# Kernel tuning notes

Hardware: AMD Instinct MI355X
Metric: run time of the kernel (lower is better)

Reference implementation:

```python
import jax, jax.numpy as jnp
import numpy as np

B, S, D, H, DH = 2, 2048, 1024, 16, 64  # batch, seq, d_hidden, n_head, d_head


def setup_inputs() -> dict:
    key = jax.random.key(0)
    ks = jax.random.split(key, 11)
    sc = 0.02
    inp = {
        "Q": jax.random.normal(ks[0], (B, S, D), jnp.float32),
        "K": jax.random.normal(ks[1], (B, S, D), jnp.float32),
        "V": jax.random.normal(ks[2], (B, S, D), jnp.float32),
        # causal mask: True = masked (strictly upper triangular), broadcast to [B,S,S]
        "attn_mask": jnp.broadcast_to(jnp.triu(jnp.ones((S, S), bool), k=1), (B, S, S)),
        "W_q": jax.random.normal(ks[3], (H * DH, D), jnp.float32) * sc,
        "b_q": jnp.zeros((H * DH,), jnp.float32),
        "W_k": jax.random.normal(ks[4], (H * DH, D), jnp.float32) * sc,
        "b_k": jnp.zeros((H * DH,), jnp.float32),
        "W_v": jax.random.normal(ks[5], (H * DH, D), jnp.float32) * sc,
        "b_v": jnp.zeros((H * DH,), jnp.float32),
        "W_o": jax.random.normal(ks[6], (D, H * DH), jnp.float32) * sc,
        "b_o": jnp.zeros((D,), jnp.float32),
    }
    return inp


def reference(Q, K, V, attn_mask, W_q, b_q, W_k, b_k, W_v, b_v, W_o, b_o):
    scaler = 1.0 / (DH ** 0.5)
    # projections: torch Linear is x @ W.T + b
    def proj(x, W, b):
        y = jnp.einsum('bsd,ed->bse', x, W) + b  # e = H*DH
        return y.reshape(x.shape[0], x.shape[1], H, DH).transpose(0, 2, 1, 3)  # [B,H,S,DH]
    q = proj(Q, W_q, b_q)
    k = proj(K, W_k, b_k)
    v = proj(V, W_v, b_v)
    score = jnp.einsum('bhqd,bhkd->bhqk', q, k) * scaler
    score = jnp.where(attn_mask[:, None, :, :], jnp.float32(-1e9), score)
    attn_prob = jax.nn.softmax(score, axis=-1)  # dropout p=0.0 -> identity
    context = jnp.einsum('bhqk,bhkd->bhqd', attn_prob, v)
    context = context.transpose(0, 2, 1, 3).reshape(Q.shape[0], -1, H * DH)
    output = jnp.einsum('bse,de->bsd', context, W_o) + b_o
    return (output, attn_prob)
```

## Files before the change

kernel.cpp:

```cpp
#include <hip/hip_runtime.h>
#include <hip/hip_bf16.h>

typedef __attribute__((ext_vector_type(8))) __bf16 bf16x8;
typedef __attribute__((ext_vector_type(4))) float f32x4;
typedef __attribute__((ext_vector_type(4))) float f4;

#define MB 2
#define MS 2048
#define MD 1024
#define MH 16
#define MDH 64

__device__ __forceinline__ void gl_lds16(const __bf16* g, __bf16* l) {
  __builtin_amdgcn_global_load_lds(
      (const __attribute__((address_space(1))) unsigned int*)g,
      (__attribute__((address_space(3))) unsigned int*)l, 16, 0, 0);
}

__device__ __forceinline__ void stage64(const __bf16* __restrict__ g, int gstride,
                                        __bf16* lds, int t) {
#pragma unroll
  for (int j = 0; j < 2; j++) {
    const int slot = t + j * 256;
    const int r = slot >> 3;
    const int c = (slot & 7) ^ (r & 7);
    gl_lds16(g + (size_t)r * gstride + c * 8, &lds[slot * 8]);
  }
}

__device__ __forceinline__ bf16x8 frag_ld(const __bf16* lds, int row, int kc) {
  const int slot = row * 8 + (kc ^ (row & 7));
  return *(const bf16x8*)&lds[slot * 8];
}

__global__ __launch_bounds__(256) void convert_kernel(
    const float* __restrict__ Q, const float* __restrict__ K, const float* __restrict__ V,
    const float* __restrict__ Wq, const float* __restrict__ Wk, const float* __restrict__ Wv,
    const float* __restrict__ Wo, __bf16* __restrict__ Ab, __bf16* __restrict__ Wb) {
  const size_t base = ((size_t)blockIdx.x * 256 + threadIdx.x) * 8;
  const float* src;
  __bf16* dst;
  size_t off;
  if (base < 3UL * 4194304UL) {
    const int z = (int)(base >> 22);
    off = base & 4194303UL;
    src = (z == 0) ? Q : ((z == 1) ? K : V);
    dst = Ab + ((size_t)z << 22);
  } else {
    const size_t b2 = base - 3UL * 4194304UL;
    const int w = (int)(b2 >> 20);
    off = b2 & 1048575UL;
    src = (w == 0) ? Wq : ((w == 1) ? Wk : ((w == 2) ? Wv : Wo));
    dst = Wb + ((size_t)w << 20);
  }
  f4 a = *(const f4*)(src + off);
  f4 b = *(const f4*)(src + off + 4);
  bf16x8 o;
#pragma unroll
  for (int j = 0; j < 4; j++) {
    o[j] = (__bf16)a[j];
    o[j + 4] = (__bf16)b[j];
  }
  *(bf16x8*)(dst + off) = o;
}

__device__ __forceinline__ void gemm_core(const __bf16* __restrict__ A,
                                          const __bf16* __restrict__ W,
                                          int tile_m, int tile_n,
                                          f32x4 acc[4][4]) {
  __shared__ __bf16 a_lds[8192];
  __shared__ __bf16 w_lds[8192];
  const int t = threadIdx.x;
  const int lane = t & 63, wave = t >> 6;
  const int l15 = lane & 15, quad = lane >> 4;
  const int wr = wave >> 1, wc = wave & 1;

  const f32x4 fzero = {0.f, 0.f, 0.f, 0.f};
#pragma unroll
  for (int mi = 0; mi < 4; mi++)
#pragma unroll
    for (int ni = 0; ni < 4; ni++) acc[mi][ni] = fzero;

  const __bf16* Abase = A + (size_t)(tile_m * 128) * 1024;
  const __bf16* Wbase = W + (size_t)(tile_n * 128) * 1024;

  for (int k0 = 0; k0 < 1024; k0 += 64) {
    __syncthreads();
#pragma unroll
    for (int j = 0; j < 4; j++) {
      const int slot = t + j * 256;
      const int r = slot >> 3;
      const int c = (slot & 7) ^ (r & 7);
      gl_lds16(Abase + (size_t)r * 1024 + k0 + c * 8, &a_lds[slot * 8]);
    }
#pragma unroll
    for (int j = 0; j < 4; j++) {
      const int slot = t + j * 256;
      const int r = slot >> 3;
      const int c = (slot & 7) ^ (r & 7);
      gl_lds16(Wbase + (size_t)r * 1024 + k0 + c * 8, &w_lds[slot * 8]);
    }
    __syncthreads();

#pragma unroll
    for (int kk = 0; kk < 2; kk++) {
      bf16x8 af[4], bf[4];
#pragma unroll
      for (int mi = 0; mi < 4; mi++)
        af[mi] = frag_ld(a_lds, wr * 64 + mi * 16 + l15, kk * 4 + quad);
#pragma unroll
      for (int ni = 0; ni < 4; ni++)
        bf[ni] = frag_ld(w_lds, wc * 64 + ni * 16 + l15, kk * 4 + quad);
#pragma unroll
      for (int mi = 0; mi < 4; mi++)
#pragma unroll
        for (int ni = 0; ni < 4; ni++)
          acc[mi][ni] = __builtin_amdgcn_mfma_f32_16x16x32_bf16(af[mi], bf[ni], acc[mi][ni], 0, 0, 0);
    }
  }
}

__global__ __launch_bounds__(256) void qkv_proj(
    const __bf16* __restrict__ Ab, const __bf16* __restrict__ Wb,
    const float* __restrict__ bq, const float* __restrict__ bk, const float* __restrict__ bv,
    __bf16* __restrict__ qo, __bf16* __restrict__ ko, __bf16* __restrict__ vo) {
  const int z = blockIdx.z;
  const __bf16* A = Ab + ((size_t)z << 22);
  const __bf16* W = Wb + ((size_t)z << 20);
  const float* bias = (z == 0) ? bq : ((z == 1) ? bk : bv);
  __bf16* out = (z == 0) ? qo : ((z == 1) ? ko : vo);

  f32x4 acc[4][4];
  gemm_core(A, W, blockIdx.y, blockIdx.x, acc);

  const int t = threadIdx.x;
  const int lane = t & 63, wave = t >> 6;
  const int l15 = lane & 15, quad = lane >> 4;
  const int wr = wave >> 1, wc = wave & 1;
  const float scale = (z == 0) ? 0.125f : 1.0f;

#pragma unroll
  for (int ni = 0; ni < 4; ni++) {
    const int e = blockIdx.x * 128 + wc * 64 + ni * 16 + l15;
    const float bias_v = bias[e];
    const int h = e >> 6, dh = e & 63;
#pragma unroll
    for (int mi = 0; mi < 4; mi++) {
#pragma unroll
      for (int r = 0; r < 4; r++) {
        const int sg = blockIdx.y * 128 + wr * 64 + mi * 16 + quad * 4 + r;
        const int bb = sg >> 11, s = sg & 2047;
        const float val = (acc[mi][ni][r] + bias_v) * scale;
        size_t addr;
        if (z < 2) addr = ((size_t)((bb * 16 + h) * 2048 + s)) * 64 + dh;
        else       addr = ((size_t)((bb * 16 + h) * 64 + dh)) * 2048 + s;
        out[addr] = (__bf16)val;
      }
    }
  }
}

__device__ __forceinline__ void qk_tile(const __bf16* kl, const bf16x8 qf0, const bf16x8 qf1,
                                        int l15, int quad, f32x4 sc[4]) {
  const f32x4 fzero = {0.f, 0.f, 0.f, 0.f};
#pragma unroll
  for (int blk = 0; blk < 4; blk++) {
    bf16x8 kf0 = frag_ld(kl, blk * 16 + l15, quad);
    bf16x8 kf1 = frag_ld(kl, blk * 16 + l15, 4 + quad);
    f32x4 z = fzero;
    z = __builtin_amdgcn_mfma_f32_16x16x32_bf16(qf0, kf0, z, 0, 0, 0);
    z = __builtin_amdgcn_mfma_f32_16x16x32_bf16(qf1, kf1, z, 0, 0, 0);
    sc[blk] = z;
  }
}

__device__ __forceinline__ void sm_update(const f32x4 sc[4], int kt, int q0, int wave,
                                          int quad, int l15, float m[4], float l[4],
                                          bool diag) {
#pragma unroll
  for (int r = 0; r < 4; r++) {
    const int qrow = q0 + wave * 16 + quad * 4 + r;
    float sv[4];
    float nm = m[r];
#pragma unroll
    for (int blk = 0; blk < 4; blk++) {
      const int kcol = kt * 64 + blk * 16 + l15;
      float s = sc[blk][r];
      if (diag) s = (kcol > qrow) ? -1e30f : s;
      sv[blk] = s;
      nm = fmaxf(nm, s);
    }
    float acc = l[r] * __expf(m[r] - nm);
#pragma unroll
    for (int blk = 0; blk < 4; blk++) acc += __expf(sv[blk] - nm);
    l[r] = acc;
    m[r] = nm;
  }
}

__device__ __forceinline__ void p_emit(const f32x4 sc[4], bool diag, int kt, int q0,
                                       int wave, int quad, int l15,
                                       const float m[4], const float rl[4],
                                       float* __restrict__ Pbase, __bf16* p_lds) {
#pragma unroll
  for (int r = 0; r < 4; r++) {
    const int rr = quad * 4 + r;
    const int qrow = q0 + wave * 16 + rr;
#pragma unroll
    for (int blk = 0; blk < 4; blk++) {
      const int kcol = kt * 64 + blk * 16 + l15;
      float s = sc[blk][r];
      if (diag) s = (kcol > qrow) ? -1e30f : s;
      const float p = __expf(s - m[r]) * rl[r];
      Pbase[(size_t)(wave * 16 + rr) * 2048 + kcol] = p;
      const int cc = blk * 16 + l15;
      const int sch = (cc >> 3) ^ (rr & 7);
      p_lds[wave * 1024 + rr * 64 + sch * 8 + (cc & 7)] = (__bf16)p;
    }
  }
}

__global__ __launch_bounds__(256) void attn_kernel(
    const __bf16* __restrict__ q, const __bf16* __restrict__ k,
    const __bf16* __restrict__ vt, float* __restrict__ P, __bf16* __restrict__ ctx) {
  const int lin = blockIdx.x + 32 * (blockIdx.y + 16 * blockIdx.z);
  const int x8 = lin & 7, j = lin >> 3;
  const int bh = x8 + 8 * (j & 3);
  const int qt = 31 - (j >> 2);
  const int b = bh >> 4, h = bh & 15;
  const int t = threadIdx.x;
  const int lane = t & 63, wave = t >> 6;
  const int l15 = lane & 15, quad = lane >> 4;
  const int q0 = qt * 64;

  __shared__ __bf16 sbuf[4][4096];
  __shared__ __bf16 p_lds[4096];

  const __bf16* qbase = q + ((size_t)bh * 2048 + q0) * 64;
  const __bf16* kbase = k + (size_t)bh * 2048 * 64;
  const __bf16* vbase = vt + (size_t)bh * 64 * 2048;
  float* Pbase = P + ((size_t)bh * 2048 + q0) * 2048;

  stage64(qbase, 64, sbuf[0], t);
  __syncthreads();
  const bf16x8 qf0 = frag_ld(sbuf[0], wave * 16 + l15, quad);
  const bf16x8 qf1 = frag_ld(sbuf[0], wave * 16 + l15, 4 + quad);
  __syncthreads();

  float m[4], l[4];
#pragma unroll
  for (int r = 0; r < 4; r++) { m[r] = -1e30f; l[r] = 0.f; }

  stage64(kbase, 64, sbuf[0], t);
  if (qt >= 1) stage64(kbase + 4096, 64, sbuf[1], t);
  __syncthreads();
  for (int kt0 = 0; kt0 <= qt; kt0 += 2) {
    const int pb = (kt0 & 2);
    const int nx = kt0 + 2;
    if (nx <= qt) {
      stage64(kbase + (size_t)nx * 4096, 64, sbuf[2 - pb], t);
      if (nx + 1 <= qt) stage64(kbase + (size_t)(nx + 1) * 4096, 64, sbuf[3 - pb], t);
    }
    f32x4 sc[4];
    __builtin_amdgcn_s_setprio(1);
    qk_tile(sbuf[pb], qf0, qf1, l15, quad, sc);
    __builtin_amdgcn_s_setprio(0);
    if (kt0 == qt) sm_update(sc, kt0, q0, wave, quad, l15, m, l, true);
    else           sm_update(sc, kt0, q0, wave, quad, l15, m, l, false);
    if (kt0 + 1 <= qt) {
      __builtin_amdgcn_s_setprio(1);
      qk_tile(sbuf[pb + 1], qf0, qf1, l15, quad, sc);
      __builtin_amdgcn_s_setprio(0);
      if (kt0 + 1 == qt) sm_update(sc, kt0 + 1, q0, wave, quad, l15, m, l, true);
      else               sm_update(sc, kt0 + 1, q0, wave, quad, l15, m, l, false);
    }
    __syncthreads();
  }

  float rl[4];
#pragma unroll
  for (int r = 0; r < 4; r++) {
    float mm = m[r], ll = l[r];
#pragma unroll
    for (int msk = 1; msk < 16; msk <<= 1) {
      const float mo = __shfl_xor(mm, msk, 64);
      const float lo = __shfl_xor(ll, msk, 64);
      const float mn = fmaxf(mm, mo);
      ll = ll * __expf(mm - mn) + lo * __expf(mo - mn);
      mm = mn;
    }
    m[r] = mm;
    rl[r] = 1.0f / ll;
  }

  const f32x4 fzero = {0.f, 0.f, 0.f, 0.f};
  f32x4 o[4];
#pragma unroll
  for (int d = 0; d < 4; d++) o[d] = fzero;

  stage64(kbase, 64, sbuf[0], t);
  stage64(vbase, 2048, sbuf[2], t);
  __syncthreads();
  for (int kt = 0; kt <= qt; kt++) {
    const int cb = kt & 1;
    if (kt < qt) {
      stage64(kbase + (size_t)(kt + 1) * 4096, 64, sbuf[cb ^ 1], t);
      stage64(vbase + (size_t)(kt + 1) * 64, 2048, sbuf[2 + (cb ^ 1)], t);
    }
    f32x4 sc[4];
    __builtin_amdgcn_s_setprio(1);
    qk_tile(sbuf[cb], qf0, qf1, l15, quad, sc);
    __builtin_amdgcn_s_setprio(0);

    if (kt == qt) p_emit(sc, true, kt, q0, wave, quad, l15, m, rl, Pbase, p_lds);
    else          p_emit(sc, false, kt, q0, wave, quad, l15, m, rl, Pbase, p_lds);

    const bf16x8 pf0 = *(const bf16x8*)&p_lds[wave * 1024 + l15 * 64 + ((quad ^ (l15 & 7)) << 3)];
    const bf16x8 pf1 = *(const bf16x8*)&p_lds[wave * 1024 + l15 * 64 + (((4 + quad) ^ (l15 & 7)) << 3)];
    __builtin_amdgcn_s_setprio(1);
#pragma unroll
    for (int d = 0; d < 4; d++) {
      bf16x8 vf0 = frag_ld(sbuf[2 + cb], d * 16 + l15, quad);
      bf16x8 vf1 = frag_ld(sbuf[2 + cb], d * 16 + l15, 4 + quad);
      o[d] = __builtin_amdgcn_mfma_f32_16x16x32_bf16(pf0, vf0, o[d], 0, 0, 0);
      o[d] = __builtin_amdgcn_mfma_f32_16x16x32_bf16(pf1, vf1, o[d], 0, 0, 0);
    }
    __builtin_amdgcn_s_setprio(0);
    __syncthreads();
  }

  const int c0 = (qt + 1) * 64;
  const int zr = t >> 2;
  for (int c = c0 + (t & 3) * 4; c < 2048; c += 16)
    *(f32x4*)&Pbase[(size_t)zr * 2048 + c] = fzero;

#pragma unroll
  for (int d = 0; d < 4; d++) {
#pragma unroll
    for (int r = 0; r < 4; r++) {
      const int sl = wave * 16 + quad * 4 + r;
      const size_t idx = ((size_t)(b * 2048 + q0 + sl)) * 1024 + h * 64 + d * 16 + l15;
      ctx[idx] = (__bf16)o[d][r];
    }
  }
}

__global__ __launch_bounds__(256) void out_proj(
    const __bf16* __restrict__ ctxp, const __bf16* __restrict__ Wob,
    const float* __restrict__ bo, float* __restrict__ out) {
  f32x4 acc[4][4];
  gemm_core(ctxp, Wob, blockIdx.y, blockIdx.x, acc);

  const int t = threadIdx.x;
  const int lane = t & 63, wave = t >> 6;
  const int l15 = lane & 15, quad = lane >> 4;
  const int wr = wave >> 1, wc = wave & 1;

#pragma unroll
  for (int ni = 0; ni < 4; ni++) {
    const int e = blockIdx.x * 128 + wc * 64 + ni * 16 + l15;
    const float bias_v = bo[e];
#pragma unroll
    for (int mi = 0; mi < 4; mi++) {
#pragma unroll
      for (int r = 0; r < 4; r++) {
        const int sg = blockIdx.y * 128 + wr * 64 + mi * 16 + quad * 4 + r;
        out[(size_t)sg * 1024 + e] = acc[mi][ni][r] + bias_v;
      }
    }
  }
}

extern "C" void kernel_launch(void* const* d_in, const int* in_sizes, int n_in,
                              void* d_out, int out_size, void* d_ws, size_t ws_size,
                              hipStream_t stream) {
  const float* Q  = (const float*)d_in[0];
  const float* K  = (const float*)d_in[1];
  const float* V  = (const float*)d_in[2];
  const float* Wq = (const float*)d_in[4];
  const float* bq = (const float*)d_in[5];
  const float* Wk = (const float*)d_in[6];
  const float* bk = (const float*)d_in[7];
  const float* Wv = (const float*)d_in[8];
  const float* bv = (const float*)d_in[9];
  const float* Wo = (const float*)d_in[10];
  const float* bo = (const float*)d_in[11];

  float* out0 = (float*)d_out;
  float* P = out0 + (size_t)MB * MS * MD;

  __bf16* Ab  = (__bf16*)d_ws;
  __bf16* Wb  = Ab + 3UL * 4194304UL;
  __bf16* qws = Wb + 4UL * 1048576UL;
  __bf16* kws = qws + 4194304UL;
  __bf16* vws = kws + 4194304UL;
  __bf16* cws = vws + 4194304UL;

  convert_kernel<<<dim3(8192), 256, 0, stream>>>(Q, K, V, Wq, Wk, Wv, Wo, Ab, Wb);
  qkv_proj<<<dim3(8, 32, 3), 256, 0, stream>>>(Ab, Wb, bq, bk, bv, qws, kws, vws);
  attn_kernel<<<dim3(32, 16, 2), 256, 0, stream>>>(qws, kws, vws, P, cws);
  out_proj<<<dim3(8, 32, 1), 256, 0, stream>>>(cws, Wb + 3UL * 1048576UL, bo, out0);
}
```

Baseline: 773.0 us.

## Double-buffer GEMM LDS staging, remap GEMM tiles per XCD, use nontemporal P stores

The shared GEMM core now double-buffers its LDS tiles, issuing the next K-slice's global-to-LDS loads before computing on the current one, so each iteration needs one barrier instead of two. The QKV and output projection launches are flattened to 1D grids and remapped so that consecutive tiles sharing A rows land on the same XCD, which is meant to improve L2 reuse. The attention-probability writes, including the zero fill of the masked region, become nontemporal stores to reduce cache pollution from the large P output. LDS use per GEMM block doubles, which may lower occupancy, and an unused xcd_remap helper is left in the code.

New measurement: 823.3 us. 6.5% more time.

```diff
diff --git a/kernel.cpp b/kernel.cpp
--- a/kernel.cpp
+++ b/kernel.cpp
@@ -25,6 +25,17 @@
     const int r = slot >> 3;
     const int c = (slot & 7) ^ (r & 7);
     gl_lds16(g + (size_t)r * gstride + c * 8, &lds[slot * 8]);
+  }
+}
+
+__device__ __forceinline__ void stage128(const __bf16* __restrict__ base, int k0,
+                                         __bf16* lds, int t) {
+#pragma unroll
+  for (int j = 0; j < 4; j++) {
+    const int slot = t + j * 256;
+    const int r = slot >> 3;
+    const int c = (slot & 7) ^ (r & 7);
+    gl_lds16(base + (size_t)r * 1024 + k0 + c * 8, &lds[slot * 8]);
   }
 }
 
@@ -68,8 +79,8 @@
                                           const __bf16* __restrict__ W,
                                           int tile_m, int tile_n,
                                           f32x4 acc[4][4]) {
-  __shared__ __bf16 a_lds[8192];
-  __shared__ __bf16 w_lds[8192];
+  __shared__ __bf16 a_lds[2][8192];
+  __shared__ __bf16 w_lds[2][8192];
   const int t = threadIdx.x;
   const int lane = t & 63, wave = t >> 6;
   const int l15 = lane & 15, quad = lane >> 4;
@@ -84,54 +95,62 @@
   const __bf16* Abase = A + (size_t)(tile_m * 128) * 1024;
   const __bf16* Wbase = W + (size_t)(tile_n * 128) * 1024;
 
+  stage128(Abase, 0, a_lds[0], t);
+  stage128(Wbase, 0, w_lds[0], t);
+  __syncthreads();
+
+  int cur = 0;
   for (int k0 = 0; k0 < 1024; k0 += 64) {
-    __syncthreads();
-#pragma unroll
-    for (int j = 0; j < 4; j++) {
-      const int slot = t + j * 256;
-      const int r = slot >> 3;
-      const int c = (slot & 7) ^ (r & 7);
-      gl_lds16(Abase + (size_t)r * 1024 + k0 + c * 8, &a_lds[slot * 8]);
-    }
-#pragma unroll
-    for (int j = 0; j < 4; j++) {
-      const int slot = t + j * 256;
-      const int r = slot >> 3;
-      const int c = (slot & 7) ^ (r & 7);
-      gl_lds16(Wbase + (size_t)r * 1024 + k0 + c * 8, &w_lds[slot * 8]);
-    }
-    __syncthreads();
-
+    if (k0 + 64 < 1024) {
+      stage128(Abase, k0 + 64, a_lds[cur ^ 1], t);
+      stage128(Wbase, k0 + 64, w_lds[cur ^ 1], t);
+    }
 #pragma unroll
     for (int kk = 0; kk < 2; kk++) {
       bf16x8 af[4], bf[4];
 #pragma unroll
       for (int mi = 0; mi < 4; mi++)
-        af[mi] = frag_ld(a_lds, wr * 64 + mi * 16 + l15, kk * 4 + quad);
+        af[mi] = frag_ld(a_lds[cur], wr * 64 + mi * 16 + l15, kk * 4 + quad);
 #pragma unroll
       for (int ni = 0; ni < 4; ni++)
-        bf[ni] = frag_ld(w_lds, wc * 64 + ni * 16 + l15, kk * 4 + quad);
+        bf[ni] = frag_ld(w_lds[cur], wc * 64 + ni * 16 + l15, kk * 4 + quad);
 #pragma unroll
       for (int mi = 0; mi < 4; mi++)
 #pragma unroll
         for (int ni = 0; ni < 4; ni++)
           acc[mi][ni] = __builtin_amdgcn_mfma_f32_16x16x32_bf16(af[mi], bf[ni], acc[mi][ni], 0, 0, 0);
     }
-  }
+    __syncthreads();
+    cur ^= 1;
+  }
+}
+
+__device__ __forceinline__ void xcd_remap(int lin, int nrow_per_z, int& x, int& y, int& z) {
+  const int c = lin & 7;
+  const int m = lin >> 3;
+  z = m / (nrow_per_z * 8 / 8);
+  (void)nrow_per_z; (void)c; (void)x; (void)y;
 }
 
 __global__ __launch_bounds__(256) void qkv_proj(
     const __bf16* __restrict__ Ab, const __bf16* __restrict__ Wb,
     const float* __restrict__ bq, const float* __restrict__ bk, const float* __restrict__ bv,
     __bf16* __restrict__ qo, __bf16* __restrict__ ko, __bf16* __restrict__ vo) {
-  const int z = blockIdx.z;
+  const int lin = blockIdx.x;
+  const int c = lin & 7;
+  const int m = lin >> 3;
+  const int z = m >> 5;
+  const int m2 = m & 31;
+  const int ty = c * 4 + (m2 >> 3);
+  const int tx = m2 & 7;
+
   const __bf16* A = Ab + ((size_t)z << 22);
   const __bf16* W = Wb + ((size_t)z << 20);
   const float* bias = (z == 0) ? bq : ((z == 1) ? bk : bv);
   __bf16* out = (z == 0) ? qo : ((z == 1) ? ko : vo);
 
   f32x4 acc[4][4];
-  gemm_core(A, W, blockIdx.y, blockIdx.x, acc);
+  gemm_core(A, W, ty, tx, acc);
 
   const int t = threadIdx.x;
   const int lane = t & 63, wave = t >> 6;
@@ -141,14 +160,14 @@
 
 #pragma unroll
   for (int ni = 0; ni < 4; ni++) {
-    const int e = blockIdx.x * 128 + wc * 64 + ni * 16 + l15;
+    const int e = tx * 128 + wc * 64 + ni * 16 + l15;
     const float bias_v = bias[e];
     const int h = e >> 6, dh = e & 63;
 #pragma unroll
     for (int mi = 0; mi < 4; mi++) {
 #pragma unroll
       for (int r = 0; r < 4; r++) {
-        const int sg = blockIdx.y * 128 + wr * 64 + mi * 16 + quad * 4 + r;
+        const int sg = ty * 128 + wr * 64 + mi * 16 + quad * 4 + r;
         const int bb = sg >> 11, s = sg & 2047;
         const float val = (acc[mi][ni][r] + bias_v) * scale;
         size_t addr;
@@ -212,7 +231,7 @@
       float s = sc[blk][r];
       if (diag) s = (kcol > qrow) ? -1e30f : s;
       const float p = __expf(s - m[r]) * rl[r];
-      Pbase[(size_t)(wave * 16 + rr) * 2048 + kcol] = p;
+      __builtin_nontemporal_store(p, &Pbase[(size_t)(wave * 16 + rr) * 2048 + kcol]);
       const int cc = blk * 16 + l15;
       const int sch = (cc >> 3) ^ (rr & 7);
       p_lds[wave * 1024 + rr * 64 + sch * 8 + (cc & 7)] = (__bf16)p;
@@ -332,7 +351,7 @@
   const int c0 = (qt + 1) * 64;
   const int zr = t >> 2;
   for (int c = c0 + (t & 3) * 4; c < 2048; c += 16)
-    *(f32x4*)&Pbase[(size_t)zr * 2048 + c] = fzero;
+    __builtin_nontemporal_store(fzero, (f32x4*)&Pbase[(size_t)zr * 2048 + c]);
 
 #pragma unroll
   for (int d = 0; d < 4; d++) {
@@ -348,8 +367,14 @@
 __global__ __launch_bounds__(256) void out_proj(
     const __bf16* __restrict__ ctxp, const __bf16* __restrict__ Wob,
     const float* __restrict__ bo, float* __restrict__ out) {
+  const int lin = blockIdx.x;
+  const int c = lin & 7;
+  const int m = lin >> 3;
+  const int ty = c * 4 + (m >> 3);
+  const int tx = m & 7;
+
   f32x4 acc[4][4];
-  gemm_core(ctxp, Wob, blockIdx.y, blockIdx.x, acc);
+  gemm_core(ctxp, Wob, ty, tx, acc);
 
   const int t = threadIdx.x;
   const int lane = t & 63, wave = t >> 6;
@@ -358,13 +383,13 @@
 
 #pragma unroll
   for (int ni = 0; ni < 4; ni++) {
-    const int e = blockIdx.x * 128 + wc * 64 + ni * 16 + l15;
+    const int e = tx * 128 + wc * 64 + ni * 16 + l15;
     const float bias_v = bo[e];
 #pragma unroll
     for (int mi = 0; mi < 4; mi++) {
 #pragma unroll
       for (int r = 0; r < 4; r++) {
-        const int sg = blockIdx.y * 128 + wr * 64 + mi * 16 + quad * 4 + r;
+        const int sg = ty * 128 + wr * 64 + mi * 16 + quad * 4 + r;
         out[(size_t)sg * 1024 + e] = acc[mi][ni][r] + bias_v;
       }
     }
@@ -397,7 +422,7 @@
   __bf16* cws = vws + 4194304UL;
 
   convert_kernel<<<dim3(8192), 256, 0, stream>>>(Q, K, V, Wq, Wk, Wv, Wo, Ab, Wb);
-  qkv_proj<<<dim3(8, 32, 3), 256, 0, stream>>>(Ab, Wb, bq, bk, bv, qws, kws, vws);
+  qkv_proj<<<dim3(768), 256, 0, stream>>>(Ab, Wb, bq, bk, bv, qws, kws, vws);
   attn_kernel<<<dim3(32, 16, 2), 256, 0, stream>>>(qws, kws, vws, P, cws);
-  out_proj<<<dim3(8, 32, 1), 256, 0, stream>>>(cws, Wb + 3UL * 1048576UL, bo, out0);
-}
+  out_proj<<<dim3(256), 256, 0, stream>>>(cws, Wb + 3UL * 1048576UL, bo, out0);
+}
```
